# Optimization experiments

Measured on AMD Instinct MI355X. Metric: run time of the kernel, lower is better.

Reference implementation:

```python
import jax, jax.numpy as jnp
import numpy as np

B, NF, FD, ND, C, K, L = 32, 64, 64, 256, 8, 6, 2  # batch, num_frames(feat), fused_dim, nodes, edge channels, neighbors, layers


def setup_inputs() -> dict:
    key = jax.random.key(0)
    ks = jax.random.split(key, 6)
    s = lambda k, shape: jax.random.normal(k, shape, jnp.float32) * 0.05
    return {
        "fused": jax.random.normal(ks[0], (B, NF, FD), jnp.float32),
        "w1": s(ks[1], (NF, FD, FD)),
        "b1": jnp.zeros((NF, 1, FD), jnp.float32),
        "w2": s(ks[2], (NF, FD, ND)),
        "b2": jnp.zeros((NF, 1, ND), jnp.float32),
        "edge_qk_w": s(ks[3], (2 * C * NF, NF)),
        "ga_qk_w": s(ks[4], (L, 2 * NF, NF)),
        "ga_qk_b": jnp.zeros((L, 2 * NF), jnp.float32),
        "ga_w": jnp.ones((L, 1, C), jnp.float32),
    }


def _spec_norm(w):
    # per-node spectral normalization (torch does this in-place under no_grad)
    n = jax.lax.stop_gradient(jnp.linalg.norm(w, ord=2, axis=(1, 2), keepdims=True))
    return w / jnp.clip(n, 1e-6, None)


def _forward(fused, w1, b1, w2, b2, edge_qk_w, ga_qk_w, ga_qk_b, ga_w):
    scale = NF ** -0.5
    # --- MultiNodeMlp (per-frame node-wise MLP) ---
    h = jnp.einsum('bni,nij->bnj', fused, _spec_norm(w1)) + b1[:, 0]
    h = jax.nn.gelu(h, approximate=False)
    conv = jnp.einsum('bni,nio->bno', h, _spec_norm(w2)) + b2[:, 0]  # [B,NF,ND]
    x = conv.transpose(0, 2, 1)  # node features [B,ND,NF]

    # --- EdgeLayer: multi-channel attention + top-k clip + double normalization ---
    qk = (x @ edge_qk_w.T).reshape(B, ND, 2, C, NF)
    q = qk[:, :, 0].transpose(0, 2, 1, 3)  # [B,C,ND,NF]
    k = qk[:, :, 1].transpose(0, 2, 1, 3)
    attn = jax.nn.softmax(jnp.einsum('bcnf,bcmf->bcnm', q, k) * scale, axis=-1)
    sum_edge = jax.lax.stop_gradient(attn).sum(axis=1)            # [B,ND,ND]
    top_idx = jax.lax.top_k(sum_edge, K)[1]                       # [B,ND,K]
    onehot = jnp.clip(jax.nn.one_hot(top_idx, ND, dtype=attn.dtype).sum(axis=2), 0.0, 1.0)
    mask = jnp.maximum(onehot, jnp.eye(ND, dtype=attn.dtype))[:, None]  # [B,1,ND,ND]
    masked = mask * attn
    nr = masked / (masked.sum(-1, keepdims=True) + 1e-6)
    nc = nr / (nr.sum(-2, keepdims=True) + 1e-6)
    edge = jnp.einsum('bcnd,bcmd->bcnm', nr, nc)                  # norm_row @ norm_col^T

    # --- LipschitzGraph: residual invertible graph attention layers ---
    eye = jnp.eye(NF, dtype=x.dtype)
    for l in range(L):
        W, bqk, wch = ga_qk_w[l], ga_qk_b[l], ga_w[l]
        xs = jax.nn.sigmoid(jax.nn.elu(x))
        qkx = xs @ W.T + bqk                                       # [B,ND,2NF]
        qg, kg = qkx[..., :NF], qkx[..., NF:]
        a = jax.nn.softmax(jnp.einsum('bnf,bmf->bnm', qg, kg) * scale, axis=-1)
        ne = a[:, None] * edge                                     # [B,C,ND,ND]
        ne = ne / (ne.sum(-1, keepdims=True) + 1e-6)
        ne = jnp.einsum('bcnd,c->bnd', ne, (wch / wch.sum())[0])
        dot = W[:NF] @ W[NF:].T * scale
        lip = jax.lax.stop_gradient(jnp.linalg.norm(eye + 2.0 * dot, ord=2)) + 5.0
        x = x + (ne @ xs) / lip
    return x


def reference(fused, w1, b1, w2, b2, edge_qk_w, ga_qk_w, ga_qk_b, ga_w):
    return _forward(fused, w1, b1, w2, b2, edge_qk_w, ga_qk_w, ga_qk_b, ga_w)
```

## Files before the change

### kernel.cpp

```cpp
#include <hip/hip_runtime.h>
#include <float.h>
#include <math.h>


typedef short bf8t __attribute__((ext_vector_type(8)));
typedef float f4t __attribute__((ext_vector_type(4)));

static __device__ __forceinline__ unsigned short f2bf(float x) {
  union { float f; unsigned u; } v; v.f = x;
  unsigned r = (v.u + 0x7FFFu + ((v.u >> 16) & 1u)) >> 16;
  return (unsigned short)r;
}
static __device__ __forceinline__ float bf2f(unsigned short s) {
  union { unsigned u; float f; } v; v.u = ((unsigned)s) << 16; return v.f;
}
static __device__ __forceinline__ float bf2f_lo(unsigned u) {
  union { unsigned u; float f; } v; v.u = u << 16; return v.f;
}
static __device__ __forceinline__ float bf2f_hi(unsigned u) {
  union { unsigned u; float f; } v; v.u = u & 0xFFFF0000u; return v.f;
}
static __device__ __forceinline__ float dot3_pair(unsigned uqh, unsigned uql,
                                                  unsigned ukh, unsigned ukl) {
  float s = bf2f_lo(uqh) * (bf2f_lo(ukh) + bf2f_lo(ukl)) + bf2f_lo(uql) * bf2f_lo(ukh);
  s += bf2f_hi(uqh) * (bf2f_hi(ukh) + bf2f_hi(ukl)) + bf2f_hi(uql) * bf2f_hi(ukh);
  return s;
}
static __device__ __forceinline__ void split8(const float* __restrict__ p,
                                              bf8t* hi, bf8t* lo) {
  float4 v0 = *(const float4*)(p);
  float4 v1 = *(const float4*)(p + 4);
  float v[8] = {v0.x, v0.y, v0.z, v0.w, v1.x, v1.y, v1.z, v1.w};
#pragma unroll
  for (int j = 0; j < 8; j++) {
    unsigned short h = f2bf(v[j]);
    (*hi)[j] = (short)h;
    (*lo)[j] = (short)f2bf(v[j] - bf2f(h));
  }
}

#define SPAD 68

static __device__ __forceinline__ void mm_mfma(
    const float* __restrict__ A, const float* __restrict__ B,
    float* __restrict__ C, int t, float scale, int addI, int transposeStore) {
  int wv = t >> 6, l = t & 63;
  int m16 = l & 15, quad = l >> 4;
  bf8t ah[2], al[2];
  const float* ap = A + (size_t)(16 * wv + m16) * SPAD + quad * 8;
  split8(ap, &ah[0], &al[0]);
  split8(ap + 32, &ah[1], &al[1]);
  f4t acc[4];
#pragma unroll
  for (int ct = 0; ct < 4; ct++) {
    bf8t bh[2], bl[2];
    const float* bp = B + (size_t)(ct * 16 + m16) * SPAD + quad * 8;
    split8(bp, &bh[0], &bl[0]);
    split8(bp + 32, &bh[1], &bl[1]);
    f4t a = (f4t){0.f, 0.f, 0.f, 0.f};
    a = __builtin_amdgcn_mfma_f32_16x16x32_bf16(al[0], bh[0], a, 0, 0, 0);
    a = __builtin_amdgcn_mfma_f32_16x16x32_bf16(ah[0], bl[0], a, 0, 0, 0);
    a = __builtin_amdgcn_mfma_f32_16x16x32_bf16(ah[0], bh[0], a, 0, 0, 0);
    a = __builtin_amdgcn_mfma_f32_16x16x32_bf16(al[1], bh[1], a, 0, 0, 0);
    a = __builtin_amdgcn_mfma_f32_16x16x32_bf16(ah[1], bl[1], a, 0, 0, 0);
    a = __builtin_amdgcn_mfma_f32_16x16x32_bf16(ah[1], bh[1], a, 0, 0, 0);
    acc[ct] = a;
  }
#pragma unroll
  for (int ct = 0; ct < 4; ct++)
#pragma unroll
    for (int j = 0; j < 4; j++) {
      int i0 = 16 * wv + quad * 4 + j;
      int j0 = ct * 16 + m16;
      float v = acc[ct][j] * scale + ((addI && i0 == j0) ? 1.0f : 0.0f);
      if (transposeStore) C[(size_t)j0 * SPAD + i0] = v;
      else C[(size_t)i0 * SPAD + j0] = v;
    }
}

static __device__ __forceinline__ void mm_sq_norm(
    const float* __restrict__ A, float* __restrict__ C, int t,
    float* __restrict__ redm) {
  int wv = t >> 6, l = t & 63;
  int m16 = l & 15, quad = l >> 4;
  bf8t ah[2], al[2];
  const float* ap = A + (size_t)(16 * wv + m16) * SPAD + quad * 8;
  split8(ap, &ah[0], &al[0]);
  split8(ap + 32, &ah[1], &al[1]);
  f4t acc[4];
#pragma unroll
  for (int ct = 0; ct < 4; ct++) {
    bf8t bh[2], bl[2];
    const float* bp = A + (size_t)(ct * 16 + m16) * SPAD + quad * 8;
    split8(bp, &bh[0], &bl[0]);
    split8(bp + 32, &bh[1], &bl[1]);
    f4t a = (f4t){0.f, 0.f, 0.f, 0.f};
    a = __builtin_amdgcn_mfma_f32_16x16x32_bf16(al[0], bh[0], a, 0, 0, 0);
    a = __builtin_amdgcn_mfma_f32_16x16x32_bf16(ah[0], bl[0], a, 0, 0, 0);
    a = __builtin_amdgcn_mfma_f32_16x16x32_bf16(ah[0], bh[0], a, 0, 0, 0);
    a = __builtin_amdgcn_mfma_f32_16x16x32_bf16(al[1], bh[1], a, 0, 0, 0);
    a = __builtin_amdgcn_mfma_f32_16x16x32_bf16(ah[1], bl[1], a, 0, 0, 0);
    a = __builtin_amdgcn_mfma_f32_16x16x32_bf16(ah[1], bh[1], a, 0, 0, 0);
    acc[ct] = a;
  }
  float mx = 0.f;
#pragma unroll
  for (int ct = 0; ct < 4; ct++)
#pragma unroll
    for (int j = 0; j < 4; j++) mx = fmaxf(mx, fabsf(acc[ct][j]));
#pragma unroll
  for (int m = 1; m < 64; m <<= 1) mx = fmaxf(mx, __shfl_xor(mx, m, 64));
  if (l == 0) redm[wv] = mx;
  __syncthreads();
  float gmx = fmaxf(fmaxf(redm[0], redm[1]), fmaxf(redm[2], redm[3]));
  float sc = 1.0f / fmaxf(gmx, 1e-30f);
#pragma unroll
  for (int ct = 0; ct < 4; ct++)
#pragma unroll
    for (int j = 0; j < 4; j++)
      C[(size_t)(16 * wv + quad * 4 + j) * SPAD + ct * 16 + m16] = acc[ct][j] * sc;
}

static __device__ __forceinline__ void gram_mfma(
    const float* __restrict__ Ag, int ncols, float* __restrict__ S,
    float* __restrict__ G, int t) {
  int wv = t >> 6, l = t & 63;
  int m16 = l & 15, quad = l >> 4;
  f4t acc[4];
#pragma unroll
  for (int ct = 0; ct < 4; ct++) acc[ct] = (f4t){0.f, 0.f, 0.f, 0.f};
  for (int cc = 0; cc < ncols; cc += 64) {
    if (cc) __syncthreads();
    for (int i = t; i < 1024; i += 256) {
      int r = i >> 4, qq = i & 15;
      float4 v = *(const float4*)(Ag + (size_t)r * ncols + cc + 4 * qq);
      *(float4*)(S + (size_t)r * SPAD + 4 * qq) = v;
    }
    __syncthreads();
    bf8t ah[2], al[2];
    const float* ap = S + (size_t)(16 * wv + m16) * SPAD + quad * 8;
    split8(ap, &ah[0], &al[0]);
    split8(ap + 32, &ah[1], &al[1]);
#pragma unroll
    for (int ct = 0; ct < 4; ct++) {
      bf8t bh[2], bl[2];
      const float* bp = S + (size_t)(ct * 16 + m16) * SPAD + quad * 8;
      split8(bp, &bh[0], &bl[0]);
      split8(bp + 32, &bh[1], &bl[1]);
      f4t a = acc[ct];
      a = __builtin_amdgcn_mfma_f32_16x16x32_bf16(al[0], bh[0], a, 0, 0, 0);
      a = __builtin_amdgcn_mfma_f32_16x16x32_bf16(ah[0], bl[0], a, 0, 0, 0);
      a = __builtin_amdgcn_mfma_f32_16x16x32_bf16(ah[0], bh[0], a, 0, 0, 0);
      a = __builtin_amdgcn_mfma_f32_16x16x32_bf16(al[1], bh[1], a, 0, 0, 0);
      a = __builtin_amdgcn_mfma_f32_16x16x32_bf16(ah[1], bl[1], a, 0, 0, 0);
      a = __builtin_amdgcn_mfma_f32_16x16x32_bf16(ah[1], bh[1], a, 0, 0, 0);
      acc[ct] = a;
    }
  }
  __syncthreads();
#pragma unroll
  for (int ct = 0; ct < 4; ct++)
#pragma unroll
    for (int j = 0; j < 4; j++)
      G[(size_t)(16 * wv + quad * 4 + j) * SPAD + ct * 16 + m16] = acc[ct][j];
}

static __device__ __forceinline__ float power_rayleigh(
    const float* __restrict__ G4m, const float* __restrict__ Gm, int iters, int i) {
  float row[64];
#pragma unroll
  for (int j = 0; j < 16; j++)
    *(float4*)(row + 4 * j) = *(const float4*)(G4m + (size_t)i * SPAD + 4 * j);
  float v = 1.0f + 0.3f * sinf(7.0f * (float)(i + 1));
  for (int it = 0; it < iters; it++) {
    float u0 = 0.f, u1 = 0.f, u2 = 0.f, u3 = 0.f;
#pragma unroll
    for (int j = 0; j < 16; j++) {
      u0 += row[4 * j + 0] * __shfl(v, 4 * j + 0, 64);
      u1 += row[4 * j + 1] * __shfl(v, 4 * j + 1, 64);
      u2 += row[4 * j + 2] * __shfl(v, 4 * j + 2, 64);
      u3 += row[4 * j + 3] * __shfl(v, 4 * j + 3, 64);
    }
    float u = (u0 + u1) + (u2 + u3);
    float ss = u * u;
#pragma unroll
    for (int m = 1; m < 64; m <<= 1) ss += __shfl_xor(ss, m, 64);
    v = u * rsqrtf(fmaxf(ss, 1e-30f));
  }
  float rowg[64];
#pragma unroll
  for (int j = 0; j < 16; j++)
    *(float4*)(rowg + 4 * j) = *(const float4*)(Gm + (size_t)i * SPAD + 4 * j);
  float u0 = 0.f, u1 = 0.f, u2 = 0.f, u3 = 0.f;
#pragma unroll
  for (int j = 0; j < 16; j++) {
    u0 += rowg[4 * j + 0] * __shfl(v, 4 * j + 0, 64);
    u1 += rowg[4 * j + 1] * __shfl(v, 4 * j + 1, 64);
    u2 += rowg[4 * j + 2] * __shfl(v, 4 * j + 2, 64);
    u3 += rowg[4 * j + 3] * __shfl(v, 4 * j + 3, 64);
  }
  float u = (u0 + u1) + (u2 + u3);
  float d = v * u;
#pragma unroll
  for (int m = 1; m < 64; m <<= 1) d += __shfl_xor(d, m, 64);
  return d;
}

__global__ __launch_bounds__(256) void speclip_kernel(
    const float* __restrict__ w1, const float* __restrict__ w2,
    const float* __restrict__ gaw, float* __restrict__ invsig1,
    float* __restrict__ invsig2, float* __restrict__ lipv) {
  __shared__ float Sa[64 * SPAD];
  __shared__ float Sb[64 * SPAD];
  __shared__ float G[64 * SPAD];
  __shared__ float redm[4];
  int t = threadIdx.x;
  int blk = blockIdx.x;
  if (blk < 128) {
    int n = blk & 63;
    const float* A = (blk < 64) ? (w1 + (size_t)n * 4096) : (w2 + (size_t)n * 16384);
    int ncols = (blk < 64) ? 64 : 256;
    gram_mfma(A, ncols, Sa, G, t);
    __syncthreads();
    mm_mfma(G, G, Sa, t, 1.f, 0, 0);
    __syncthreads();
    mm_sq_norm(Sa, Sb, t, redm);  __syncthreads();
    mm_sq_norm(Sb, Sa, t, redm);  __syncthreads();
    mm_sq_norm(Sa, Sb, t, redm);  __syncthreads();
    mm_sq_norm(Sb, Sa, t, redm);  __syncthreads();
    mm_sq_norm(Sa, Sb, t, redm);  __syncthreads();
    mm_sq_norm(Sb, Sa, t, redm);  __syncthreads();
    if (t < 64) {
      float d = power_rayleigh(Sa, G, 2, t);
      if (t == 0) {
        float sg = sqrtf(fmaxf(d, 0.f));
        float inv = 1.0f / fmaxf(sg, 1e-6f);
        if (blk < 64) invsig1[n] = inv; else invsig2[n] = inv;
      }
    }
  } else {
    int l = blk - 128;
    const float* Wb = gaw + (size_t)l * 8192;
    for (int i = t; i < 1024; i += 256) {
      int r = i >> 4, qq = i & 15;
      *(float4*)(Sa + (size_t)r * SPAD + 4 * qq) = *(const float4*)(Wb + r * 64 + 4 * qq);
      *(float4*)(Sb + (size_t)r * SPAD + 4 * qq) = *(const float4*)(Wb + 4096 + r * 64 + 4 * qq);
    }
    __syncthreads();
    mm_mfma(Sa, Sb, G, t, 0.25f, 1, 1);
    __syncthreads();
    mm_mfma(G, G, Sa, t, 1.f, 0, 0);
    __syncthreads();
    mm_sq_norm(Sa, Sb, t, redm);  __syncthreads();
    mm_sq_norm(Sb, G, t, redm);   __syncthreads();
    mm_sq_norm(G, Sb, t, redm);   __syncthreads();
    mm_sq_norm(Sb, G, t, redm);   __syncthreads();
    mm_sq_norm(G, Sb, t, redm);   __syncthreads();
    mm_sq_norm(Sb, G, t, redm);   __syncthreads();
    if (t < 64) {
      float d = power_rayleigh(G, Sa, 2, t);
      if (t == 0) lipv[l] = sqrtf(fmaxf(d, 0.f)) + 5.0f;
    }
  }
}

__global__ __launch_bounds__(256) void h_kernel(
    const float* __restrict__ fused, const float* __restrict__ w1,
    const float* __restrict__ b1, const float* __restrict__ invsig1,
    float* __restrict__ h) {
  __shared__ float fr[256];
  int t = threadIdx.x;
  int blk = blockIdx.x;
  int ng = blk & 15;
  fr[t] = fused[(size_t)blk * 256 + t];
  __syncthreads();
  int nl = t >> 6, j = t & 63;
  int n = ng * 4 + nl;
  float is1 = invsig1[n];
  const float* fp = fr + nl * 64;
  const float* wp = w1 + (size_t)n * 4096 + j;
  float acc = 0.f;
  for (int i = 0; i < 64; i++) acc += fp[i] * wp[i * 64];
  acc = acc * is1 + b1[n * 64 + j];
  float g = 0.5f * acc * (1.0f + erff(acc * 0.70710678118654752440f));
  h[(size_t)blk * 256 + t] = g;
}

__global__ __launch_bounds__(256) void conv_kernel(
    const float* __restrict__ h, const float* __restrict__ w2,
    const float* __restrict__ b2, const float* __restrict__ invsig2,
    float* __restrict__ x) {
  __shared__ float hr[4][64];
  int t = threadIdx.x;
  int blk = blockIdx.x;
  int b = blk >> 4, ng = blk & 15;
  int n0 = ng * 4;
  {
    int r = t >> 6, i = t & 63;
    hr[r][i] = h[((size_t)b * 64 + n0 + r) * 64 + i];
  }
  __syncthreads();
  const float* w0p = w2 + ((size_t)(n0 + 0) * 64) * 256 + t;
  const float* w1p = w2 + ((size_t)(n0 + 1) * 64) * 256 + t;
  const float* w2p = w2 + ((size_t)(n0 + 2) * 64) * 256 + t;
  const float* w3p = w2 + ((size_t)(n0 + 3) * 64) * 256 + t;
  float a0 = 0.f, a1 = 0.f, a2 = 0.f, a3 = 0.f;
  for (int i = 0; i < 64; i++) {
    a0 += hr[0][i] * w0p[(size_t)i * 256];
    a1 += hr[1][i] * w1p[(size_t)i * 256];
    a2 += hr[2][i] * w2p[(size_t)i * 256];
    a3 += hr[3][i] * w3p[(size_t)i * 256];
  }
  float4 o;
  o.x = a0 * invsig2[n0 + 0] + b2[(n0 + 0) * 256 + t];
  o.y = a1 * invsig2[n0 + 1] + b2[(n0 + 1) * 256 + t];
  o.z = a2 * invsig2[n0 + 2] + b2[(n0 + 2) * 256 + t];
  o.w = a3 * invsig2[n0 + 3] + b2[(n0 + 3) * 256 + t];
  *(float4*)(x + ((size_t)b * 256 + t) * 64 + n0) = o;
}

__global__ __launch_bounds__(256, 2) void qk_kernel(
    const float* __restrict__ x, const float* __restrict__ eqk,
    unsigned short* __restrict__ qhi, unsigned short* __restrict__ qlo,
    unsigned short* __restrict__ khi, unsigned short* __restrict__ klo) {
  int t = threadIdx.x;
  int blk = blockIdx.x;
  int xcd = blk & 7;
  int y = blk >> 3;
  int rh = y & 1;
  int c = (y >> 1) & 7;
  int b = (y >> 4) * 8 + xcd;
  int wv = t >> 6, l = t & 63;
  int m16 = l & 15, quad = l >> 4;
  int row0 = rh * 128 + wv * 32;

  bf8t ah[2][2], al[2][2];
#pragma unroll
  for (int rt = 0; rt < 2; rt++) {
    const float* xp = x + ((size_t)b * 256 + row0 + rt * 16 + m16) * 64 + quad * 8;
    split8(xp, &ah[rt][0], &al[rt][0]);
    split8(xp + 32, &ah[rt][1], &al[rt][1]);
  }
#pragma unroll
  for (int mat = 0; mat < 2; mat++) {
    const float* Wbase = eqk + ((size_t)(mat * 8 + c) * 64) * 64;
    unsigned short* ohi = mat ? khi : qhi;
    unsigned short* olo = mat ? klo : qlo;
#pragma unroll
    for (int ct = 0; ct < 4; ct++) {
      bf8t bh[2], bl[2];
      const float* wp = Wbase + (size_t)(ct * 16 + m16) * 64 + quad * 8;
      split8(wp, &bh[0], &bl[0]);
      split8(wp + 32, &bh[1], &bl[1]);
#pragma unroll
      for (int rt = 0; rt < 2; rt++) {
        f4t a = (f4t){0.f, 0.f, 0.f, 0.f};
        a = __builtin_amdgcn_mfma_f32_16x16x32_bf16(al[rt][0], bh[0], a, 0, 0, 0);
        a = __builtin_amdgcn_mfma_f32_16x16x32_bf16(ah[rt][0], bl[0], a, 0, 0, 0);
        a = __builtin_amdgcn_mfma_f32_16x16x32_bf16(ah[rt][0], bh[0], a, 0, 0, 0);
        a = __builtin_amdgcn_mfma_f32_16x16x32_bf16(al[rt][1], bh[1], a, 0, 0, 0);
        a = __builtin_amdgcn_mfma_f32_16x16x32_bf16(ah[rt][1], bl[1], a, 0, 0, 0);
        a = __builtin_amdgcn_mfma_f32_16x16x32_bf16(ah[rt][1], bh[1], a, 0, 0, 0);
#pragma unroll
        for (int j = 0; j < 4; j++) {
          int n = row0 + rt * 16 + quad * 4 + j;
          int f = ct * 16 + m16;
          size_t o = (((size_t)b * 8 + c) * 256 + n) * 64 + f;
          float v = a[j];
          unsigned short hh = f2bf(v);
          ohi[o] = hh;
          olo[o] = f2bf(v - bf2f(hh));
        }
      }
    }
  }
}

__global__ __launch_bounds__(256, 2) void transpose_kernel(
    const float* __restrict__ in, float* __restrict__ out) {
  __shared__ float T[256 * 65];
  int t = threadIdx.x;
  size_t base = (size_t)blockIdx.x * 16384;
  const float4* in4 = (const float4*)(in + base);
  float4* out4 = (float4*)(out + base);
  for (int i = t; i < 4096; i += 256) {
    int n = i >> 4, fq = i & 15;
    float4 v = in4[i];
    float* dst = T + n * 65 + 4 * fq;
    dst[0] = v.x; dst[1] = v.y; dst[2] = v.z; dst[3] = v.w;
  }
  __syncthreads();
  for (int i = t; i < 4096; i += 256) {
    int f = i >> 6, m4 = i & 63;
    float4 o;
    o.x = T[(4 * m4 + 0) * 65 + f];
    o.y = T[(4 * m4 + 1) * 65 + f];
    o.z = T[(4 * m4 + 2) * 65 + f];
    o.w = T[(4 * m4 + 3) * 65 + f];
    out4[f * 64 + m4] = o;
  }
}

__global__ __launch_bounds__(512, 4) void attn_kernel(
    const unsigned short* __restrict__ qhi, const unsigned short* __restrict__ qlo,
    const unsigned short* __restrict__ khi, const unsigned short* __restrict__ klo,
    float* __restrict__ seP, float* __restrict__ mxb, float* __restrict__ rzb) {
  __shared__ float sE[32 * 260];
  int t = threadIdx.x;
  int blk = blockIdx.x;
  int xcd = blk & 7;
  int y = blk >> 3;
  int b = xcd * 4 + (y & 3);
  int cg = (y >> 2) & 3;
  int ng = y >> 4;
  int wave = t >> 6;
  int ci = wave >> 2;
  int wv = wave & 3;
  int l = t & 63;
  int m16 = l & 15, quad = l >> 4;
  int n0w = ng * 64 + wv * 16;
  int c = cg * 2 + ci;

  size_t sl = ((size_t)b * 8 + c) * 16384;
  const bf8t* qh = (const bf8t*)(qhi + sl + (size_t)(n0w + m16) * 64 + quad * 8);
  const bf8t* ql = (const bf8t*)(qlo + sl + (size_t)(n0w + m16) * 64 + quad * 8);
  bf8t ah0 = qh[0], ah1 = qh[4];
  bf8t al0 = ql[0], al1 = ql[4];
  f4t acc[16];
#pragma unroll
  for (int mt = 0; mt < 16; mt++) acc[mt] = (f4t){0.f, 0.f, 0.f, 0.f};
  for (int mt = 0; mt < 16; mt++) {
    const bf8t* kh = (const bf8t*)(khi + sl + (size_t)(mt * 16 + m16) * 64 + quad * 8);
    const bf8t* kl = (const bf8t*)(klo + sl + (size_t)(mt * 16 + m16) * 64 + quad * 8);
    bf8t bh0 = kh[0], bh1 = kh[4];
    bf8t bl0 = kl[0], bl1 = kl[4];
    f4t a = acc[mt];
    a = __builtin_amdgcn_mfma_f32_16x16x32_bf16(al0, bh0, a, 0, 0, 0);
    a = __builtin_amdgcn_mfma_f32_16x16x32_bf16(ah0, bl0, a, 0, 0, 0);
    a = __builtin_amdgcn_mfma_f32_16x16x32_bf16(ah0, bh0, a, 0, 0, 0);
    a = __builtin_amdgcn_mfma_f32_16x16x32_bf16(al1, bh1, a, 0, 0, 0);
    a = __builtin_amdgcn_mfma_f32_16x16x32_bf16(ah1, bl1, a, 0, 0, 0);
    a = __builtin_amdgcn_mfma_f32_16x16x32_bf16(ah1, bh1, a, 0, 0, 0);
    acc[mt] = a;
  }
#pragma unroll
  for (int j = 0; j < 4; j++) {
    float mx = -FLT_MAX;
#pragma unroll
    for (int mt = 0; mt < 16; mt++) mx = fmaxf(mx, acc[mt][j]);
    mx = fmaxf(mx, __shfl_xor(mx, 1, 64));
    mx = fmaxf(mx, __shfl_xor(mx, 2, 64));
    mx = fmaxf(mx, __shfl_xor(mx, 4, 64));
    mx = fmaxf(mx, __shfl_xor(mx, 8, 64));
    float mxl = mx * 0.125f;
    float z = 0.f;
#pragma unroll
    for (int mt = 0; mt < 16; mt++) {
      float e = expf(acc[mt][j] * 0.125f - mxl);
      acc[mt][j] = e;
      z += e;
    }
    z += __shfl_xor(z, 1, 64);
    z += __shfl_xor(z, 2, 64);
    z += __shfl_xor(z, 4, 64);
    z += __shfl_xor(z, 8, 64);
    int n = n0w + quad * 4 + j;
    if (m16 == 0) {
      mxb[((size_t)b * 8 + c) * 256 + n] = mxl;
      rzb[((size_t)b * 8 + c) * 256 + n] = z;
    }
    float zi = 1.0f / z;
#pragma unroll
    for (int mt = 0; mt < 16; mt++) acc[mt][j] *= zi;
  }
  for (int half = 0; half < 2; half++) {
    if (ci == 0 && (wv >> 1) == half) {
      int r0 = (wv & 1) * 16;
#pragma unroll
      for (int mt = 0; mt < 16; mt++)
#pragma unroll
        for (int j = 0; j < 4; j++)
          sE[(r0 + quad * 4 + j) * 260 + mt * 16 + m16] = acc[mt][j];
    }
    __syncthreads();
    if (ci == 1 && (wv >> 1) == half) {
      int r0 = (wv & 1) * 16;
#pragma unroll
      for (int mt = 0; mt < 16; mt++)
#pragma unroll
        for (int j = 0; j < 4; j++)
          sE[(r0 + quad * 4 + j) * 260 + mt * 16 + m16] += acc[mt][j];
    }
    __syncthreads();
    float4* dst4 = (float4*)(seP + (((size_t)cg * 32 + b) * 256 + ng * 64 + half * 32) * 256);
    for (int i = t; i < 2048; i += 512) {
      int r = i >> 6, c4 = i & 63;
      dst4[i] = *(const float4*)(sE + r * 260 + c4 * 4);
    }
    if (half == 0) __syncthreads();
  }
}

__global__ __launch_bounds__(256) void topsel_kernel(
    const float* __restrict__ seP, int* __restrict__ idx7) {
  __shared__ float seL[64 * 260];
  __shared__ float cv[64][24];
  __shared__ int cidx[64][24];
  int t = threadIdx.x;
  int b = blockIdx.x >> 2, rg = blockIdx.x & 3;
  int n0 = rg * 64;
  const float* s0 = seP + ((size_t)b * 256 + n0) * 256;
  const float* s1 = seP + ((size_t)(32 + b) * 256 + n0) * 256;
  const float* s2 = seP + ((size_t)(64 + b) * 256 + n0) * 256;
  const float* s3 = seP + ((size_t)(96 + b) * 256 + n0) * 256;
  for (int i = t; i < 4096; i += 256) {
    int m4 = i & 63, r = i >> 6;
    float4 v0 = ((const float4*)(s0 + (size_t)r * 256))[m4];
    float4 v1 = ((const float4*)(s1 + (size_t)r * 256))[m4];
    float4 v2 = ((const float4*)(s2 + (size_t)r * 256))[m4];
    float4 v3 = ((const float4*)(s3 + (size_t)r * 256))[m4];
    float4 s;
    s.x = (v0.x + v1.x) + (v2.x + v3.x);
    s.y = (v0.y + v1.y) + (v2.y + v3.y);
    s.z = (v0.z + v1.z) + (v2.z + v3.z);
    s.w = (v0.w + v1.w) + (v2.w + v3.w);
    *(float4*)(seL + r * 260 + m4 * 4) = s;
  }
  __syncthreads();
  {
    int r = t >> 2, qtr = t & 3;
    float tv[6]; int ti[6];
#pragma unroll
    for (int s = 0; s < 6; s++) { tv[s] = -FLT_MAX; ti[s] = 1 << 30; }
    for (int i = 0; i < 64; i++) {
      int m = 4 * i + qtr;
      float val = seL[r * 260 + m];
      if (val > tv[5]) {
        tv[5] = val; ti[5] = m;
#pragma unroll
        for (int s = 5; s > 0; s--) {
          if (tv[s] > tv[s - 1]) {
            float tmv = tv[s]; tv[s] = tv[s - 1]; tv[s - 1] = tmv;
            int tmi = ti[s]; ti[s] = ti[s - 1]; ti[s - 1] = tmi;
          }
        }
      }
    }
#pragma unroll
    for (int s = 0; s < 6; s++) { cv[r][qtr * 6 + s] = tv[s]; cidx[r][qtr * 6 + s] = ti[s]; }
  }
  __syncthreads();
  if (t < 64) {
    int r = t, n = n0 + r;
    int sel[7];
    for (int round = 0; round < 6; round++) {
      float best = -FLT_MAX; int bi = 1 << 30, bs = 0;
      for (int j = 0; j < 24; j++) {
        float v = cv[r][j]; int id = cidx[r][j];
        if (v > best || (v == best && id < bi)) { best = v; bi = id; bs = j; }
      }
      sel[round] = bi;
      cv[r][bs] = -FLT_MAX;
    }
    bool dup = false;
#pragma unroll
    for (int j = 0; j < 6; j++) dup = dup || (sel[j] == n);
    sel[6] = dup ? -1 : n;
#pragma unroll
    for (int j = 0; j < 7; j++) idx7[((size_t)b * 256 + n) * 7 + j] = sel[j];
  }
}

__global__ __launch_bounds__(256) void nr_kernel(
    const unsigned short* __restrict__ qhi, const unsigned short* __restrict__ qlo,
    const unsigned short* __restrict__ khi, const unsigned short* __restrict__ klo,
    const float* __restrict__ mxb, const float* __restrict__ rzb,
    const int* __restrict__ idx7, float* __restrict__ nrv,
    float* __restrict__ colsum) {
  __shared__ int idxs[7];
  __shared__ float attL[56];
  int t = threadIdx.x;
  int b = blockIdx.x >> 8, n = blockIdx.x & 255;
  if (t < 7) idxs[t] = idx7[(size_t)blockIdx.x * 7 + t];
  __syncthreads();
  int task = t >> 2, l4 = t & 3;
  if (task < 56) {
    int c = task / 7, j = task - c * 7;
    int d = idxs[j];
    float s = 0.f;
    if (d >= 0) {
      size_t qo = (((size_t)b * 8 + c) * 256 + n) * 64 + l4 * 16;
      size_t ko = (((size_t)b * 8 + c) * 256 + d) * 64 + l4 * 16;
      const uint4* qh4 = (const uint4*)(qhi + qo);
      const uint4* ql4 = (const uint4*)(qlo + qo);
      const uint4* kh4 = (const uint4*)(khi + ko);
      const uint4* kl4 = (const uint4*)(klo + ko);
#pragma unroll
      for (int g = 0; g < 2; g++) {
        uint4 uqh = qh4[g], uql = ql4[g], ukh = kh4[g], ukl = kl4[g];
        s += dot3_pair(uqh.x, uql.x, ukh.x, ukl.x);
        s += dot3_pair(uqh.y, uql.y, ukh.y, ukl.y);
        s += dot3_pair(uqh.z, uql.z, ukh.z, ukl.z);
        s += dot3_pair(uqh.w, uql.w, ukh.w, ukl.w);
      }
    }
    s += __shfl_xor(s, 1, 64);
    s += __shfl_xor(s, 2, 64);
    if (l4 == 0) {
      float att = 0.f;
      if (d >= 0) {
        float logit = s * 0.125f;
        att = expf(logit - mxb[((size_t)b * 8 + c) * 256 + n]) / rzb[((size_t)b * 8 + c) * 256 + n];
      }
      attL[task] = att;
    }
  }
  __syncthreads();
  if (t < 8) {
    float rs = 0.f;
#pragma unroll
    for (int j = 0; j < 7; j++) rs += attL[t * 7 + j];
    float ri = 1.0f / (rs + 1e-6f);
#pragma unroll
    for (int j = 0; j < 7; j++) {
      float nv = attL[t * 7 + j] * ri;
      nrv[(((size_t)b * 8 + t) * 256 + n) * 7 + j] = nv;
      int d = idxs[j];
      if (d >= 0) atomicAdd(&colsum[((size_t)b * 8 + t) * 256 + d], nv);
    }
  }
}

__global__ __launch_bounds__(256, 3) void edge_kernel(
    const int* __restrict__ idx7, const float* __restrict__ nrv,
    const float* __restrict__ colsum, unsigned short* __restrict__ edge) {
  __shared__ unsigned short ncT[256 * 64];
  __shared__ short idxL[256 * 8];
  __shared__ float nrvL[256 * 8];
  int t = threadIdx.x;
  int blk = blockIdx.x;
  int b = blk >> 5, c = (blk >> 2) & 7, mq = blk & 3;
  int m0 = mq * 64;
  for (int i = t; i < 8192; i += 256) ((unsigned int*)ncT)[i] = 0u;
  for (int i = t; i < 2048; i += 256) {
    int r = i >> 3, j = i & 7;
    if (j < 7) {
      idxL[i] = (short)idx7[(size_t)b * 1792 + r * 7 + j];
      nrvL[i] = nrv[((size_t)b * 8 + c) * 1792 + r * 7 + j];
    } else {
      idxL[i] = -1;
      nrvL[i] = 0.f;
    }
  }
  __syncthreads();
  for (int i = t; i < 448; i += 256) {
    int mi = i / 7, j = i - mi * 7;
    int m = m0 + mi;
    int d = idxL[m * 8 + j];
    if (d >= 0) {
      float cs = colsum[((size_t)b * 8 + c) * 256 + d];
      ncT[d * 64 + mi] = f2bf(nrvL[m * 8 + j] / (cs + 1e-6f));
    }
  }
  __syncthreads();
  int wv = t >> 6, l = t & 63;
  int half = l >> 5, p = l & 31;
  const unsigned int* ncP = (const unsigned int*)ncT;
  unsigned int* eb = (unsigned int*)(edge + (((size_t)b * 8 + c) * 256) * 256);
  for (int nn = 0; nn < 32; nn++) {
    int n = nn * 8 + wv * 2 + half;
    int4 iv = *(const int4*)(idxL + n * 8);
    float4 w0 = *(const float4*)(nrvL + n * 8);
    float4 w1 = *(const float4*)(nrvL + n * 8 + 4);
    float a0 = 0.f, a1 = 0.f;
    int d;
    unsigned int pr;
    d = (int)(short)(iv.x & 0xFFFF);
    if (d >= 0) { pr = ncP[d * 32 + p]; a0 += w0.x * bf2f_lo(pr); a1 += w0.x * bf2f_hi(pr); }
    d = iv.x >> 16;
    if (d >= 0) { pr = ncP[d * 32 + p]; a0 += w0.y * bf2f_lo(pr); a1 += w0.y * bf2f_hi(pr); }
    d = (int)(short)(iv.y & 0xFFFF);
    if (d >= 0) { pr = ncP[d * 32 + p]; a0 += w0.z * bf2f_lo(pr); a1 += w0.z * bf2f_hi(pr); }
    d = iv.y >> 16;
    if (d >= 0) { pr = ncP[d * 32 + p]; a0 += w0.w * bf2f_lo(pr); a1 += w0.w * bf2f_hi(pr); }
    d = (int)(short)(iv.z & 0xFFFF);
    if (d >= 0) { pr = ncP[d * 32 + p]; a0 += w1.x * bf2f_lo(pr); a1 += w1.x * bf2f_hi(pr); }
    d = iv.z >> 16;
    if (d >= 0) { pr = ncP[d * 32 + p]; a0 += w1.y * bf2f_lo(pr); a1 += w1.y * bf2f_hi(pr); }
    d = (int)(short)(iv.w & 0xFFFF);
    if (d >= 0) { pr = ncP[d * 32 + p]; a0 += w1.z * bf2f_lo(pr); a1 += w1.z * bf2f_hi(pr); }
    unsigned int packo = (unsigned int)f2bf(a0) | ((unsigned int)f2bf(a1) << 16);
    eb[n * 128 + (m0 >> 1) + p] = packo;
  }
}

static __device__ __forceinline__ float selu1(float v) {
  float e = (v > 0.f) ? v : expm1f(v);
  return 1.0f / (1.0f + expf(-e));
}
__global__ __launch_bounds__(256, 1) void qkx_kernel(
    const float* __restrict__ x, const float* __restrict__ gaw,
    const float* __restrict__ gab, int l, float* __restrict__ xs,
    float* __restrict__ qg, float* __restrict__ kg) {
  __shared__ float xsL[64 * 64];
  int t = threadIdx.x;
  int b = blockIdx.x >> 2, nt = blockIdx.x & 3;
  int f = t & 63, part = t >> 6;
  float wq[64], wk[64];
  const float4* Wq4 = (const float4*)(gaw + (size_t)l * 8192 + f * 64);
  const float4* Wk4 = (const float4*)(gaw + (size_t)l * 8192 + (64 + f) * 64);
#pragma unroll
  for (int j = 0; j < 16; j++) {
    float4 aa = Wq4[j];
    wq[4 * j + 0] = aa.x; wq[4 * j + 1] = aa.y; wq[4 * j + 2] = aa.z; wq[4 * j + 3] = aa.w;
    float4 bb = Wk4[j];
    wk[4 * j + 0] = bb.x; wk[4 * j + 1] = bb.y; wk[4 * j + 2] = bb.z; wk[4 * j + 3] = bb.w;
  }
  float bq = gab[l * 128 + f], bk = gab[l * 128 + 64 + f];
  for (int i = t; i < 1024; i += 256) {
    float4 v = ((const float4*)(x + ((size_t)b * 256 + nt * 64) * 64))[i];
    float4 o;
    o.x = selu1(v.x); o.y = selu1(v.y); o.z = selu1(v.z); o.w = selu1(v.w);
    ((float4*)xsL)[i] = o;
    ((float4*)(xs + ((size_t)b * 256 + nt * 64) * 64))[i] = o;
  }
  __syncthreads();
  for (int i = 0; i < 16; i++) {
    int nl = part * 16 + i;
    const float4* xr = (const float4*)(xsL + nl * 64);
    float aq = 0.f, ak = 0.f;
#pragma unroll
    for (int j = 0; j < 16; j++) {
      float4 v = xr[j];
      aq += v.x * wq[4 * j] + v.y * wq[4 * j + 1] + v.z * wq[4 * j + 2] + v.w * wq[4 * j + 3];
      ak += v.x * wk[4 * j] + v.y * wk[4 * j + 1] + v.z * wk[4 * j + 2] + v.w * wk[4 * j + 3];
    }
    int n = nt * 64 + nl;
    qg[((size_t)b * 256 + n) * 64 + f] = aq + bq;
    kg[((size_t)b * 256 + n) * 64 + f] = ak + bk;
  }
}

__global__ __launch_bounds__(256, 2) void ga_attn_kernel(
    const float* __restrict__ qg, const float* __restrict__ kgT,
    float* __restrict__ a) {
  int t = threadIdx.x;
  int b = blockIdx.x >> 3, nt = blockIdx.x & 7;
  int n0 = nt * 32;
  int wv = t >> 6, l = t & 63;
  const float* kb = kgT + (size_t)b * 16384 + 4 * l;
  const float* qb = qg + ((size_t)b * 256 + n0 + wv * 8) * 64;
  float acc[8][4];
#pragma unroll
  for (int r = 0; r < 8; r++)
#pragma unroll
    for (int j = 0; j < 4; j++) acc[r][j] = 0.f;
#pragma unroll 4
  for (int kq4 = 0; kq4 < 64; kq4 += 4) {
    float4 kv0 = *(const float4*)(kb + (kq4 + 0) * 256);
    float4 kv1 = *(const float4*)(kb + (kq4 + 1) * 256);
    float4 kv2 = *(const float4*)(kb + (kq4 + 2) * 256);
    float4 kv3 = *(const float4*)(kb + (kq4 + 3) * 256);
#pragma unroll
    for (int r = 0; r < 8; r++) {
      float4 qv = *(const float4*)(qb + r * 64 + kq4);
      acc[r][0] += qv.x * kv0.x + qv.y * kv1.x + qv.z * kv2.x + qv.w * kv3.x;
      acc[r][1] += qv.x * kv0.y + qv.y * kv1.y + qv.z * kv2.y + qv.w * kv3.y;
      acc[r][2] += qv.x * kv0.z + qv.y * kv1.z + qv.z * kv2.z + qv.w * kv3.z;
      acc[r][3] += qv.x * kv0.w + qv.y * kv1.w + qv.z * kv2.w + qv.w * kv3.w;
    }
  }
#pragma unroll
  for (int r = 0; r < 8; r++) {
    float l0 = acc[r][0] * 0.125f, l1 = acc[r][1] * 0.125f;
    float l2 = acc[r][2] * 0.125f, l3 = acc[r][3] * 0.125f;
    float mx = fmaxf(fmaxf(l0, l1), fmaxf(l2, l3));
#pragma unroll
    for (int m = 1; m < 64; m <<= 1) mx = fmaxf(mx, __shfl_xor(mx, m, 64));
    float e0 = expf(l0 - mx), e1 = expf(l1 - mx), e2 = expf(l2 - mx), e3 = expf(l3 - mx);
    float z = e0 + e1 + e2 + e3;
#pragma unroll
    for (int m = 1; m < 64; m <<= 1) z += __shfl_xor(z, m, 64);
    float zi = 1.0f / z;
    int n = n0 + wv * 8 + r;
    float4 o;
    o.x = e0 * zi; o.y = e1 * zi; o.z = e2 * zi; o.w = e3 * zi;
    ((float4*)(a + ((size_t)b * 256 + n) * 256))[l] = o;
  }
}

__global__ __launch_bounds__(256) void upd_kernel(
    const float* __restrict__ a, const unsigned short* __restrict__ edge,
    const float* __restrict__ xs, const float* __restrict__ gaww,
    const float* __restrict__ lipv, int l, float* __restrict__ x) {
  __shared__ float tt[4][8][260];
  __shared__ float ne3[4][256];
  __shared__ float parts[4][4][64];
  __shared__ float dred[32][8];
  __shared__ float dinv[4][8];
  __shared__ float wcL[8];
  __shared__ float lipi;
  int t = threadIdx.x;
  int b = blockIdx.x >> 6, nq = blockIdx.x & 63;
  int n0 = nq * 4;
  if (t == 0) {
    float s = 0.f;
    float wtmp[8];
    for (int c = 0; c < 8; c++) { wtmp[c] = gaww[l * 8 + c]; s += wtmp[c]; }
    for (int c = 0; c < 8; c++) wcL[c] = wtmp[c] / s;
    lipi = 1.0f / lipv[l];
  }
#pragma unroll
  for (int r = 0; r < 4; r++) {
    float av = a[((size_t)b * 256 + n0 + r) * 256 + t];
#pragma unroll
    for (int c = 0; c < 8; c++)
      tt[r][c][t] = av * bf2f(edge[(((size_t)b * 8 + c) * 256 + n0 + r) * 256 + t]);
  }
  __syncthreads();
  {
    int rc = t >> 3, i = t & 7;
    int r = rc >> 3, c = rc & 7;
    float p = 0.f;
#pragma unroll
    for (int kq = 0; kq < 32; kq++) p += tt[r][c][i + 8 * kq];
    dred[rc][i] = p;
  }
  __syncthreads();
  if (t < 32) {
    float s = 0.f;
#pragma unroll
    for (int i = 0; i < 8; i++) s += dred[t][i];
    dinv[t >> 3][t & 7] = 1.0f / (s + 1e-6f);
  }
  __syncthreads();
#pragma unroll
  for (int r = 0; r < 4; r++) {
    float s = 0.f;
#pragma unroll
    for (int c = 0; c < 8; c++) s += wcL[c] * tt[r][c][t] * dinv[r][c];
    ne3[r][t] = s;
  }
  __syncthreads();
  {
    int f = t & 63, part = t >> 6;
    float a0 = 0.f, a1 = 0.f, a2 = 0.f, a3 = 0.f;
    for (int mm = 0; mm < 64; mm++) {
      int m = part * 64 + mm;
      float xv = xs[((size_t)b * 256 + m) * 64 + f];
      a0 += ne3[0][m] * xv;
      a1 += ne3[1][m] * xv;
      a2 += ne3[2][m] * xv;
      a3 += ne3[3][m] * xv;
    }
    parts[0][part][f] = a0;
    parts[1][part][f] = a1;
    parts[2][part][f] = a2;
    parts[3][part][f] = a3;
  }
  __syncthreads();
  {
    int r = t >> 6, f = t & 63;
    float dx = parts[r][0][f] + parts[r][1][f] + parts[r][2][f] + parts[r][3][f];
    x[((size_t)b * 256 + n0 + r) * 64 + f] += dx * lipi;
  }
}

extern "C" void kernel_launch(void* const* d_in, const int* in_sizes, int n_in,
                              void* d_out, int out_size, void* d_ws, size_t ws_size,
                              hipStream_t stream) {
  (void)in_sizes; (void)n_in; (void)out_size; (void)ws_size;
  const float* fused = (const float*)d_in[0];
  const float* w1 = (const float*)d_in[1];
  const float* b1 = (const float*)d_in[2];
  const float* w2 = (const float*)d_in[3];
  const float* b2 = (const float*)d_in[4];
  const float* eqk = (const float*)d_in[5];
  const float* gaw = (const float*)d_in[6];
  const float* gab = (const float*)d_in[7];
  const float* gaww = (const float*)d_in[8];
  float* x = (float*)d_out;
  char* ws = (char*)d_ws;
  size_t off = 0;
  auto alloc = [&](size_t bytes) -> char* {
    char* p = ws + off;
    off += (bytes + 1023) & ~(size_t)1023;
    return p;
  };
  float* invsig1 = (float*)alloc(64 * 4);
  float* invsig2 = (float*)alloc(64 * 4);
  float* lipv = (float*)alloc(2 * 4);
  float* h = (float*)alloc((size_t)32 * 64 * 64 * 4);
  unsigned short* qhi = (unsigned short*)alloc((size_t)32 * 8 * 256 * 64 * 2);
  unsigned short* qlo = (unsigned short*)alloc((size_t)32 * 8 * 256 * 64 * 2);
  unsigned short* khi = (unsigned short*)alloc((size_t)32 * 8 * 256 * 64 * 2);
  unsigned short* klo = (unsigned short*)alloc((size_t)32 * 8 * 256 * 64 * 2);
  char* sep_edge = alloc((size_t)4 * 32 * 256 * 256 * 4);
  float* seP = (float*)sep_edge;
  unsigned short* edge = (unsigned short*)sep_edge;
  float* mxb = (float*)alloc((size_t)65536 * 4);
  float* rzb = (float*)alloc((size_t)65536 * 4);
  int* idx7 = (int*)alloc((size_t)8192 * 7 * 4);
  float* nrv = (float*)alloc((size_t)65536 * 7 * 4);
  float* colsum = (float*)alloc((size_t)65536 * 4);
  float* xs = (float*)alloc((size_t)524288 * 4);
  float* qg = (float*)alloc((size_t)524288 * 4);
  float* kg = (float*)alloc((size_t)524288 * 4);
  float* a = (float*)alloc((size_t)32 * 256 * 256 * 4);
  float* kgT = (float*)alloc((size_t)524288 * 4);

  speclip_kernel<<<130, 256, 0, stream>>>(w1, w2, gaw, invsig1, invsig2, lipv);
  h_kernel<<<512, 256, 0, stream>>>(fused, w1, b1, invsig1, h);
  conv_kernel<<<512, 256, 0, stream>>>(h, w2, b2, invsig2, x);
  qk_kernel<<<512, 256, 0, stream>>>(x, eqk, qhi, qlo, khi, klo);
  attn_kernel<<<512, 512, 0, stream>>>(qhi, qlo, khi, klo, seP, mxb, rzb);
  hipMemsetAsync(colsum, 0, (size_t)65536 * 4, stream);
  topsel_kernel<<<128, 256, 0, stream>>>(seP, idx7);
  nr_kernel<<<8192, 256, 0, stream>>>(qhi, qlo, khi, klo, mxb, rzb, idx7, nrv, colsum);
  edge_kernel<<<1024, 256, 0, stream>>>(idx7, nrv, colsum, edge);
  for (int l = 0; l < 2; l++) {
    qkx_kernel<<<128, 256, 0, stream>>>(x, gaw, gab, l, xs, qg, kg);
    transpose_kernel<<<32, 256, 0, stream>>>(kg, kgT);
    ga_attn_kernel<<<256, 256, 0, stream>>>(qg, kgT, a);
    upd_kernel<<<2048, 256, 0, stream>>>(a, edge, xs, gaww, lipv, l, x);
  }
}
```

Baseline: 393.5 us.

## Stage K tiles in LDS cooperatively for attention score MFMA loop

The attention kernel now loads the key hi/lo bf16 tiles for both channels of a block into shared memory in two phases with coalesced 16-byte loads. Each wave then reads its MFMA operands from LDS instead of issuing strided global loads for every tile. The score shared buffer reuses the same LDS allocation, so an extra barrier is added before it is written. This removes redundant global K reads across the four waves sharing a channel, at the cost of extra barriers and LDS traffic.

Result: faster. 373.6 us (-5.1%).

```diff
diff --git a/kernel.cpp b/kernel.cpp
--- a/kernel.cpp
+++ b/kernel.cpp
@@ -405,7 +405,9 @@
     const unsigned short* __restrict__ qhi, const unsigned short* __restrict__ qlo,
     const unsigned short* __restrict__ khi, const unsigned short* __restrict__ klo,
     float* __restrict__ seP, float* __restrict__ mxb, float* __restrict__ rzb) {
-  __shared__ float sE[32 * 260];
+  __shared__ uint4 KS4[4096];
+  unsigned short* KS = (unsigned short*)KS4;
+  float* sE = (float*)KS4;
   int t = threadIdx.x;
   int blk = blockIdx.x;
   int xcd = blk & 7;
@@ -421,27 +423,62 @@
   int n0w = ng * 64 + wv * 16;
   int c = cg * 2 + ci;
 
+  size_t slA = ((size_t)b * 8 + cg * 2) * 16384;
+  size_t slB = slA + 16384;
   size_t sl = ((size_t)b * 8 + c) * 16384;
+
   const bf8t* qh = (const bf8t*)(qhi + sl + (size_t)(n0w + m16) * 64 + quad * 8);
   const bf8t* ql = (const bf8t*)(qlo + sl + (size_t)(n0w + m16) * 64 + quad * 8);
   bf8t ah0 = qh[0], ah1 = qh[4];
   bf8t al0 = ql[0], al1 = ql[4];
+
+  int sthalf = (t >> 6) & 1;
+  int tllo = (t >> 7) & 3;
+  int srcbase = tllo * 1024 + m16 * 64 + sthalf * 32 + quad * 8;
+  int dstbase = t * 8;
+
+  int lane8 = (quad * 16 + m16) * 8;
+  int cbase = ci * 16384;
+
   f4t acc[16];
 #pragma unroll
   for (int mt = 0; mt < 16; mt++) acc[mt] = (f4t){0.f, 0.f, 0.f, 0.f};
-  for (int mt = 0; mt < 16; mt++) {
-    const bf8t* kh = (const bf8t*)(khi + sl + (size_t)(mt * 16 + m16) * 64 + quad * 8);
-    const bf8t* kl = (const bf8t*)(klo + sl + (size_t)(mt * 16 + m16) * 64 + quad * 8);
-    bf8t bh0 = kh[0], bh1 = kh[4];
-    bf8t bl0 = kl[0], bl1 = kl[4];
-    f4t a = acc[mt];
-    a = __builtin_amdgcn_mfma_f32_16x16x32_bf16(al0, bh0, a, 0, 0, 0);
-    a = __builtin_amdgcn_mfma_f32_16x16x32_bf16(ah0, bl0, a, 0, 0, 0);
-    a = __builtin_amdgcn_mfma_f32_16x16x32_bf16(ah0, bh0, a, 0, 0, 0);
-    a = __builtin_amdgcn_mfma_f32_16x16x32_bf16(al1, bh1, a, 0, 0, 0);
-    a = __builtin_amdgcn_mfma_f32_16x16x32_bf16(ah1, bl1, a, 0, 0, 0);
-    a = __builtin_amdgcn_mfma_f32_16x16x32_bf16(ah1, bh1, a, 0, 0, 0);
-    acc[mt] = a;
+
+#pragma unroll
+  for (int p = 0; p < 2; p++) {
+    if (p) __syncthreads();
+    int pb = srcbase + p * 8192;
+#pragma unroll
+    for (int g = 0; g < 2; g++) {
+      const unsigned short* bhp = khi + (g ? slB : slA) + pb;
+      const unsigned short* blp = klo + (g ? slB : slA) + pb;
+      uint4 v0 = *(const uint4*)(bhp);
+      uint4 v1 = *(const uint4*)(bhp + 4096);
+      uint4 v2 = *(const uint4*)(blp);
+      uint4 v3 = *(const uint4*)(blp + 4096);
+      *(uint4*)(KS + dstbase + (g * 4 + 0) * 4096) = v0;
+      *(uint4*)(KS + dstbase + (g * 4 + 1) * 4096) = v1;
+      *(uint4*)(KS + dstbase + (g * 4 + 2) * 4096) = v2;
+      *(uint4*)(KS + dstbase + (g * 4 + 3) * 4096) = v3;
+    }
+    __syncthreads();
+#pragma unroll
+    for (int tl = 0; tl < 8; tl++) {
+      int mt = p * 8 + tl;
+      int tb = cbase + tl * 1024 + lane8;
+      bf8t bh0 = *(const bf8t*)(KS + tb);
+      bf8t bh1 = *(const bf8t*)(KS + tb + 512);
+      bf8t bl0 = *(const bf8t*)(KS + tb + 8192);
+      bf8t bl1 = *(const bf8t*)(KS + tb + 8704);
+      f4t a = acc[mt];
+      a = __builtin_amdgcn_mfma_f32_16x16x32_bf16(al0, bh0, a, 0, 0, 0);
+      a = __builtin_amdgcn_mfma_f32_16x16x32_bf16(ah0, bl0, a, 0, 0, 0);
+      a = __builtin_amdgcn_mfma_f32_16x16x32_bf16(ah0, bh0, a, 0, 0, 0);
+      a = __builtin_amdgcn_mfma_f32_16x16x32_bf16(al1, bh1, a, 0, 0, 0);
+      a = __builtin_amdgcn_mfma_f32_16x16x32_bf16(ah1, bl1, a, 0, 0, 0);
+      a = __builtin_amdgcn_mfma_f32_16x16x32_bf16(ah1, bh1, a, 0, 0, 0);
+      acc[mt] = a;
+    }
   }
 #pragma unroll
   for (int j = 0; j < 4; j++) {
@@ -473,6 +510,7 @@
 #pragma unroll
     for (int mt = 0; mt < 16; mt++) acc[mt][j] *= zi;
   }
+  __syncthreads();
   for (int half = 0; half < 2; half++) {
     if (ci == 0 && (wv >> 1) == half) {
       int r0 = (wv & 1) * 16;
```
